# Performance work log

Measured on AMD Instinct MI355X. Metric: run time of the kernel, lower is better.

The kernel has to match this reference:

```python
import jax, jax.numpy as jnp
import numpy as np

B, T, I, H = 2048, 512, 9, 56


def _lstm_layer(x, w_ih, w_hh, b_ih, b_hh):
    """Single LSTM layer, batch_first x: [B, T, in] -> [B, T, H].
    PyTorch gate order: i, f, g, o."""
    # Precompute input projections for all timesteps in one GEMM: [B, T, 4H]
    xp = jnp.einsum('bti,gi->btg', x, w_ih) + b_ih + b_hh
    xp_t = jnp.transpose(xp, (1, 0, 2))  # [T, B, 4H]
    h0 = jnp.zeros((x.shape[0], w_hh.shape[1]), dtype=x.dtype)
    c0 = jnp.zeros_like(h0)

    def step(carry, xt):
        h, c = carry
        gates = xt + h @ w_hh.T  # [B, 4H]
        i, f, g, o = jnp.split(gates, 4, axis=-1)
        i = jax.nn.sigmoid(i)
        f = jax.nn.sigmoid(f)
        g = jnp.tanh(g)
        o = jax.nn.sigmoid(o)
        c = f * c + i * g
        h = o * jnp.tanh(c)
        return (h, c), h

    _, hs = jax.lax.scan(step, (h0, c0), xp_t)  # hs: [T, B, H]
    return jnp.transpose(hs, (1, 0, 2))  # [B, T, H]


def setup_inputs() -> dict:
    key = jax.random.key(0)
    ks = jax.random.split(key, 13)
    s_in = 1.0 / np.sqrt(H)
    inp = {
        'x': jax.random.normal(ks[0], (B, T, I), dtype=jnp.float32),
        'w_ih0': jax.random.uniform(ks[1], (4 * H, I), jnp.float32, -s_in, s_in),
        'w_hh0': jax.random.uniform(ks[2], (4 * H, H), jnp.float32, -s_in, s_in),
        'b_ih0': jax.random.uniform(ks[3], (4 * H,), jnp.float32, -s_in, s_in),
        'b_hh0': jax.random.uniform(ks[4], (4 * H,), jnp.float32, -s_in, s_in),
        'w_ih1': jax.random.uniform(ks[5], (4 * H, H), jnp.float32, -s_in, s_in),
        'w_hh1': jax.random.uniform(ks[6], (4 * H, H), jnp.float32, -s_in, s_in),
        'b_ih1': jax.random.uniform(ks[7], (4 * H,), jnp.float32, -s_in, s_in),
        'b_hh1': jax.random.uniform(ks[8], (4 * H,), jnp.float32, -s_in, s_in),
        'fc1_w': jax.random.uniform(ks[9], (H // 2, H), jnp.float32, -s_in, s_in),
        'fc1_b': jax.random.uniform(ks[10], (H // 2,), jnp.float32, -s_in, s_in),
        'fc2_w': jax.random.uniform(ks[11], (1, H // 2), jnp.float32, -0.2, 0.2),
        'fc2_b': jax.random.uniform(ks[12], (1,), jnp.float32, -0.2, 0.2),
    }
    return inp


def reference(x, w_ih0, w_hh0, b_ih0, b_hh0, w_ih1, w_hh1, b_ih1, b_hh1,
              fc1_w, fc1_b, fc2_w, fc2_b):
    h = _lstm_layer(x, w_ih0, w_hh0, b_ih0, b_hh0)   # [B, T, H]
    h = _lstm_layer(h, w_ih1, w_hh1, b_ih1, b_hh1)   # [B, T, H]
    last = h[:, -1]                                   # [B, H]
    y = jax.nn.relu(last @ fc1_w.T + fc1_b)           # [B, H//2]
    return y @ fc2_w.T + fc2_b                        # [B, 1]
```

## Files before the change

### kernel.cpp

```cpp
#include <hip/hip_runtime.h>
#include <stdint.h>

#define T_LEN 512
#define IN0   9
#define H     56
#define BG    8
#define NW    14
#define NTH   (NW * 64)
#define NBLK  256

typedef __attribute__((ext_vector_type(8))) short bfrag;
typedef __attribute__((ext_vector_type(4))) float ffrag;

#define MFMA(a,b,c) __builtin_amdgcn_mfma_f32_16x16x32_bf16((a),(b),(c),0,0,0)

__device__ __forceinline__ uint32_t bf16hi(float x) {
  uint32_t u = __float_as_uint(x);
  return (u + 0x7FFFu + ((u >> 16) & 1u)) & 0xFFFF0000u;
}
__device__ __forceinline__ void split_bf16(float x, short& hs, short& ls) {
  uint32_t hb = bf16hi(x);
  float lf = x - __uint_as_float(hb);
  hs = (short)(hb >> 16);
  ls = (short)(bf16hi(lf) >> 16);
}
__device__ __forceinline__ void split_bf16t(float x, short& hs, short& ls) {
  uint32_t hb = bf16hi(x);
  float lf = x - __uint_as_float(hb);
  hs = (short)(hb >> 16);
  ls = (short)(__float_as_uint(lf) >> 16);
}
__device__ __forceinline__ float dpp8_add(float v) {
  int p = __builtin_amdgcn_update_dpp(0, __float_as_int(v), 0x128, 0xF, 0xF, true);
  return v + __int_as_float(p);
}
__device__ __forceinline__ float rcp_f(float v)  { return __builtin_amdgcn_rcpf(v); }
__device__ __forceinline__ float sigm_f(float v) { return rcp_f(1.0f + __expf(-v)); }
__device__ __forceinline__ float tanh_f(float v) { return 1.0f - 2.0f * rcp_f(1.0f + __expf(2.0f * v)); }

__global__ __launch_bounds__(NTH, 4)
void lstm_mfma7(const float* __restrict__ x,
                const float* __restrict__ w_ih0, const float* __restrict__ w_hh0,
                const float* __restrict__ b_ih0, const float* __restrict__ b_hh0,
                const float* __restrict__ w_ih1, const float* __restrict__ w_hh1,
                const float* __restrict__ b_ih1, const float* __restrict__ b_hh1,
                const float* __restrict__ fc1_w, const float* __restrict__ fc1_b,
                const float* __restrict__ fc2_w, const float* __restrict__ fc2_b,
                float* __restrict__ out)
{
  __shared__ __align__(16) short sB[4][1024];
  __shared__ float sF[BG * H];
  __shared__ float sY[BG * 28];

  const int tid  = threadIdx.x;
  const int lane = tid & 63;
  const int w    = tid >> 6;
  const int c16  = lane & 15;
  const int quad = lane >> 4;

  const int np   = 16 * w + c16;
  const int jb   = np >> 2, gb = np & 3;
  const int wrow = gb * H + jb;

  for (int i = tid; i < (int)(sizeof(sB) / 4); i += NTH) ((int*)sB)[i] = 0;

  bfrag B0h[2], B0l[2], Buh[2], Bhh[2];
  #pragma unroll
  for (int s = 0; s < 2; ++s) {
    union { short sh[8]; bfrag v; } a0h, a0l, auh, ahh;
    #pragma unroll
    for (int jj = 0; jj < 8; ++jj) {
      const int k = 32 * s + quad * 8 + jj;
      const float w0 = (k < H) ? w_hh0[wrow * H + k] : w_ih0[wrow * IN0 + (k - 56)];
      const float wu = (k < H) ? w_ih1[wrow * H + k] : 0.0f;
      const float wh = (k < H) ? w_hh1[wrow * H + k] : 0.0f;
      split_bf16(w0, a0h.sh[jj], a0l.sh[jj]);
      short dum;
      split_bf16(wu, auh.sh[jj], dum);
      split_bf16(wh, ahh.sh[jj], dum);
    }
    B0h[s] = a0h.v; B0l[s] = a0l.v;
    Buh[s] = auh.v; Bhh[s] = ahh.v;
  }

  const int j4 = 4 * w + quad;
  ffrag bias0f, bias1f;
  #pragma unroll
  for (int r = 0; r < 4; ++r) {
    const float v0 = b_ih0[r * H + j4] + b_hh0[r * H + j4];
    const float v1 = b_ih1[r * H + j4] + b_hh1[r * H + j4];
    bias0f[r] = (c16 < 8) ? v0 : 0.0f;
    bias1f[r] = (c16 < 8) ? v1 : 0.0f;
  }
  const ffrag zerof = { 0.f, 0.f, 0.f, 0.f };

  const int lay = (lane >> 3) & 1;
  const int b   = lane & 7;
  float wx8a[4];
  #pragma unroll
  for (int r = 0; r < 4; ++r)
    wx8a[r] = lay ? w_ih0[(r * H + j4) * IN0 + 8] : 0.0f;

  const int kk   = j4 & 31;
  const int offE = (j4 >> 5) * 512 + ((kk >> 3) * 16 + b) * 8 + (kk & 7);
  short* const hp0 = &sB[0][0] + (lay ? 0 : 3 * 1024) + offE;
  short* const hp1 = &sB[0][0] + (lay ? 1 * 1024 : 2 * 1024) + offE;

  const int shalf = lane >> 5;
  const int sbq   = (lane >> 2) & 7;
  const int sjlc  = lane & 3;
  const int offX  = 512 + (48 + sbq) * 8 + 2 * sjlc;
  short* const xst0 = &sB[0][0] + offX;
  short* const xst1 = &sB[1][0] + offX;
  const short* const sBr = &sB[0][0];

  const float* xp8 = x + (size_t)(blockIdx.x * BG + b) * T_LEN * IN0 + 8;
  const float* xps = x + (size_t)(blockIdx.x * BG + sbq) * T_LEN * IN0
                   + (size_t)w * IN0 + 2 * sjlc;

  float cst = 0.f;
  __syncthreads();

  if (w == 0 && shalf) {
    const float xa = xps[0], xb = xps[1];
    short ah, al2, bh, bl2;
    split_bf16t(xa, ah, al2); split_bf16t(xb, bh, bl2);
    *(uint32_t*)xst0        = (uint16_t)ah  | ((uint32_t)(uint16_t)bh  << 16);
    *(uint32_t*)(xst0 + 64) = (uint16_t)al2 | ((uint32_t)(uint16_t)bl2 << 16);
    xps += 2 * IN0;
  }
  __syncthreads();

  {
    bfrag U0 = *(const bfrag*)(sBr + lane * 8);
    bfrag U1 = *(const bfrag*)(sBr + 512 + lane * 8);
    ffrag a0 = MFMA(B0h[0], U0, bias0f);
    a0 = MFMA(B0h[1], U1, a0);
    a0 = MFMA(B0l[0], U0, a0);
    a0 = MFMA(B0l[1], U1, a0);
    const float x8v = xp8[0];
    xp8 += IN0;
    float s0[4];
    #pragma unroll
    for (int r = 0; r < 4; ++r) s0[r] = dpp8_add(a0[r]);
    if (lay) {
      const float gi = fmaf(wx8a[0], x8v, s0[0]);
      const float gf = fmaf(wx8a[1], x8v, s0[1]);
      const float gg = fmaf(wx8a[2], x8v, s0[2]);
      const float go = fmaf(wx8a[3], x8v, s0[3]);
      const float iv = sigm_f(gi), fv = sigm_f(gf), gv = tanh_f(gg), ov = sigm_f(go);
      cst = fmaf(fv, cst, iv * gv);
      const float hv = ov * tanh_f(cst);
      short hs, hl; split_bf16t(hv, hs, hl);
      hp1[0] = hs; hp1[64] = hl;
    }
    if (w == 1 && shalf) {
      const float xa = xps[0], xb = xps[1];
      short ah, al2, bh, bl2;
      split_bf16t(xa, ah, al2); split_bf16t(xb, bh, bl2);
      *(uint32_t*)xst1        = (uint16_t)ah  | ((uint32_t)(uint16_t)bh  << 16);
      *(uint32_t*)(xst1 + 64) = (uint16_t)al2 | ((uint32_t)(uint16_t)bl2 << 16);
      xps += 2 * IN0;
    }
    __syncthreads();
  }

#define REGION(RR, L0PART, XSTG, LASTR)                                         \
  {                                                                             \
    bfrag U0 = *(const bfrag*)(sBr + (RR ^ 1) * 1024 + lane * 8);               \
    bfrag U1 = *(const bfrag*)(sBr + (RR ^ 1) * 1024 + 512 + lane * 8);         \
    bfrag H0 = *(const bfrag*)(sBr + (2 + RR) * 1024 + lane * 8);               \
    bfrag H1 = *(const bfrag*)(sBr + (2 + RR) * 1024 + 512 + lane * 8);         \
    float x8v = 0.0f;                                                           \
    if (L0PART) { x8v = xp8[0]; xp8 += IN0; }                                   \
                                     \
    ffrag a0;                                                                   \
    if (L0PART) {                                                               \
      a0 = MFMA(B0h[0], U0, bias0f);                                            \
      a0 = MFMA(B0h[1], U1, a0);                                                \
      a0 = MFMA(B0l[0], U0, a0);                                                \
      a0 = MFMA(B0l[1], U1, a0);                                                \
    }                                                                           \
                                                 \
    ffrag aH = MFMA(Bhh[0], H0, bias1f);                                        \
    aH = MFMA(Bhh[1], H1, aH);                                                  \
    ffrag aU = MFMA(Buh[0], U0, zerof);                                         \
    aU = MFMA(Buh[1], U1, aU);                                                  \
    if (!LASTR) {                                                               \
      float sv[4];                                                              \
      _Pragma("unroll")                                                         \
      for (int r = 0; r < 4; ++r) {                                             \
        const float s1 = dpp8_add(aH[r] + aU[r]);                               \
        const float s0 = dpp8_add(a0[r]);                                       \
        sv[r] = lay ? s0 : s1;                                                  \
      }                                                                         \
      const float gi = fmaf(wx8a[0], x8v, sv[0]);                               \
      const float gf = fmaf(wx8a[1], x8v, sv[1]);                               \
      const float gg = fmaf(wx8a[2], x8v, sv[2]);                               \
      const float go = fmaf(wx8a[3], x8v, sv[3]);                               \
      const float iv = sigm_f(gi), fv = sigm_f(gf);                             \
      const float gv = tanh_f(gg), ov = sigm_f(go);                             \
      cst = fmaf(fv, cst, iv * gv);                                             \
      const float hv = ov * tanh_f(cst);                                        \
      short hs, hl; split_bf16t(hv, hs, hl);                                    \
      short* hb = (RR == 0) ? hp0 : hp1;                                        \
      hb[0] = hs; hb[64] = hl;                                                  \
    } else {                                                                    \
      float s1[4];                                                              \
      _Pragma("unroll")                                                         \
      for (int r = 0; r < 4; ++r) s1[r] = dpp8_add(aH[r] + aU[r]);              \
      if (lay == 0) {                                                           \
        const float iv = sigm_f(s1[0]), fv = sigm_f(s1[1]);                     \
        const float gv = tanh_f(s1[2]), ov = sigm_f(s1[3]);                     \
        cst = fmaf(fv, cst, iv * gv);                                           \
        sF[b * H + j4] = ov * tanh_f(cst);                                      \
      }                                                                         \
    }                                                                           \
    if (XSTG) {                                                                 \
             \
      if (w == RR && shalf) {                                                   \
        const float xa = xps[0], xb = xps[1];                                   \
        short ah, al2, bh, bl2;                                                 \
        split_bf16t(xa, ah, al2); split_bf16t(xb, bh, bl2);                     \
        short* xb_ = (RR == 0) ? xst0 : xst1;                                   \
        *(uint32_t*)xb_        = (uint16_t)ah  | ((uint32_t)(uint16_t)bh  << 16); \
        *(uint32_t*)(xb_ + 64) = (uint16_t)al2 | ((uint32_t)(uint16_t)bl2 << 16); \
        xps += 2 * IN0;                                                         \
      }                                                                         \
    }                                                                           \
    __syncthreads();                                                            \
  }

  for (int it = 0; it < 255; ++it) {
    REGION(0, 1, 1, 0)
    REGION(1, 1, 1, 0)
  }
  REGION(0, 1, 0, 0)
  REGION(1, 0, 0, 1)
#undef REGION

  if (tid < 28 * BG) {
    const int m  = tid >> 3;
    const int bb = tid & 7;
    float acc = fc1_b[m];
    const float4* w4 = (const float4*)(fc1_w + m * H);
    const float4* h4 = (const float4*)(sF + bb * H);
    #pragma unroll
    for (int qq = 0; qq < H / 4; ++qq) {
      const float4 wv4 = w4[qq], hv4 = h4[qq];
      acc = fmaf(wv4.x, hv4.x, acc);
      acc = fmaf(wv4.y, hv4.y, acc);
      acc = fmaf(wv4.z, hv4.z, acc);
      acc = fmaf(wv4.w, hv4.w, acc);
    }
    sY[bb * 28 + m] = fmaxf(acc, 0.0f);
  }
  __syncthreads();
  if (tid < BG) {
    float acc = fc2_b[0];
    #pragma unroll
    for (int m = 0; m < 28; ++m)
      acc = fmaf(fc2_w[m], sY[tid * 28 + m], acc);
    out[blockIdx.x * BG + tid] = acc;
  }
}

extern "C" void kernel_launch(void* const* d_in, const int* in_sizes, int n_in,
                              void* d_out, int out_size, void* d_ws, size_t ws_size,
                              hipStream_t stream)
{
  const float* x     = (const float*)d_in[0];
  const float* w_ih0 = (const float*)d_in[1];
  const float* w_hh0 = (const float*)d_in[2];
  const float* b_ih0 = (const float*)d_in[3];
  const float* b_hh0 = (const float*)d_in[4];
  const float* w_ih1 = (const float*)d_in[5];
  const float* w_hh1 = (const float*)d_in[6];
  const float* b_ih1 = (const float*)d_in[7];
  const float* b_hh1 = (const float*)d_in[8];
  const float* fc1_w = (const float*)d_in[9];
  const float* fc1_b = (const float*)d_in[10];
  const float* fc2_w = (const float*)d_in[11];
  const float* fc2_b = (const float*)d_in[12];
  float* out = (float*)d_out;

  lstm_mfma7<<<NBLK, NTH, 0, stream>>>(
      x, w_ih0, w_hh0, b_ih0, b_hh0, w_ih1, w_hh1, b_ih1, b_hh1,
      fc1_w, fc1_b, fc2_w, fc2_b, out);
}
```

Measured before the change: 428.3 us.

## Prestage all input timesteps into LDS before the recurrent loop

Before the time loop, each block loads all 512 timesteps of its 8 batch rows from global memory, splits them into hi/lo bf16 parts and stores them in a large LDS buffer, with the ninth input feature kept as fp32 in a separate LDS array. The recurrent steps then read the x fragment and x8 value through pointers that advance through LDS. This removes the per-step global loads and the per-step staging of x by one wave. In exchange it uses almost all of the LDS and adds a serial prologue at the start of the kernel.

```diff
diff --git a/kernel.cpp b/kernel.cpp
--- a/kernel.cpp
+++ b/kernel.cpp
@@ -39,7 +39,7 @@
 __device__ __forceinline__ float tanh_f(float v) { return 1.0f - 2.0f * rcp_f(1.0f + __expf(2.0f * v)); }
 
 __global__ __launch_bounds__(NTH, 4)
-void lstm_mfma7(const float* __restrict__ x,
+void lstm_mfma9(const float* __restrict__ x,
                 const float* __restrict__ w_ih0, const float* __restrict__ w_hh0,
                 const float* __restrict__ b_ih0, const float* __restrict__ b_hh0,
                 const float* __restrict__ w_ih1, const float* __restrict__ w_hh1,
@@ -48,7 +48,9 @@
                 const float* __restrict__ fc2_w, const float* __restrict__ fc2_b,
                 float* __restrict__ out)
 {
-  __shared__ __align__(16) short sB[4][1024];
+  __shared__ __align__(16) short hbufS[4 * 1024];
+  __shared__ __align__(16) short xfS[T_LEN * 128];
+  __shared__ __align__(16) float x8S[T_LEN * BG];
   __shared__ float sF[BG * H];
   __shared__ float sY[BG * 28];
 
@@ -62,7 +64,7 @@
   const int jb   = np >> 2, gb = np & 3;
   const int wrow = gb * H + jb;
 
-  for (int i = tid; i < (int)(sizeof(sB) / 4); i += NTH) ((int*)sB)[i] = 0;
+  for (int i = tid; i < 2048; i += NTH) ((int*)hbufS)[i] = 0;
 
   bfrag B0h[2], B0l[2], Buh[2], Bhh[2];
   #pragma unroll
@@ -103,43 +105,49 @@
 
   const int kk   = j4 & 31;
   const int offE = (j4 >> 5) * 512 + ((kk >> 3) * 16 + b) * 8 + (kk & 7);
-  short* const hp0 = &sB[0][0] + (lay ? 0 : 3 * 1024) + offE;
-  short* const hp1 = &sB[0][0] + (lay ? 1 * 1024 : 2 * 1024) + offE;
-
-  const int shalf = lane >> 5;
-  const int sbq   = (lane >> 2) & 7;
-  const int sjlc  = lane & 3;
-  const int offX  = 512 + (48 + sbq) * 8 + 2 * sjlc;
-  short* const xst0 = &sB[0][0] + offX;
-  short* const xst1 = &sB[1][0] + offX;
-  const short* const sBr = &sB[0][0];
-
-  const float* xp8 = x + (size_t)(blockIdx.x * BG + b) * T_LEN * IN0 + 8;
-  const float* xps = x + (size_t)(blockIdx.x * BG + sbq) * T_LEN * IN0
-                   + (size_t)w * IN0 + 2 * sjlc;
+  short* const hp0 = hbufS + (lay ? 0 : 3 * 1024) + offE;
+  short* const hp1 = hbufS + (lay ? 1 * 1024 : 2 * 1024) + offE;
+
+  for (int item = tid; item < T_LEN * BG; item += NTH) {
+    const int t  = item & (T_LEN - 1);
+    const int bb = item >> 9;
+    const float* xr = x + ((size_t)(blockIdx.x * BG + bb) * T_LEN + t) * IN0;
+    union { short s[8]; bfrag v; } hi, lo;
+    #pragma unroll
+    for (int q = 0; q < 8; ++q) split_bf16t(xr[q], hi.s[q], lo.s[q]);
+    *(bfrag*)((char*)xfS + (size_t)t * 256 + bb * 16)       = hi.v;
+    *(bfrag*)((char*)xfS + (size_t)t * 256 + (bb + 8) * 16) = lo.v;
+    x8S[t * 8 + bb] = xr[8];
+  }
+
+  const char* const hB = (const char*)hbufS;
+  const char* const pU0_0 = hB + 2048 + lane * 16;
+  const char* const pU0_1 = hB +        lane * 16;
+  const char* const pH0_0 = hB + 4096 + lane * 16;
+  const char* const pH1_0 = hB + 5120 + lane * 16;
+  const char* const pH0_1 = hB + 6144 + lane * 16;
+  const char* const pH1_1 = hB + 7168 + lane * 16;
+  const char* pU1_0 = (quad == 3) ? ((const char*)xfS + 256 * 1 + c16 * 16)
+                                  : (hB + 3072 + lane * 16);
+  const char* pU1_1 = (quad == 3) ? ((const char*)xfS + 256 * 2 + c16 * 16)
+                                  : (hB + 1024 + lane * 16);
+  const char* px8_0 = (const char*)x8S + 32 * 1 + b * 4;
+  const char* px8_1 = (const char*)x8S + 32 * 2 + b * 4;
+  const int incU1 = (quad == 3) ? 512 : 0;
 
   float cst = 0.f;
   __syncthreads();
 
-  if (w == 0 && shalf) {
-    const float xa = xps[0], xb = xps[1];
-    short ah, al2, bh, bl2;
-    split_bf16t(xa, ah, al2); split_bf16t(xb, bh, bl2);
-    *(uint32_t*)xst0        = (uint16_t)ah  | ((uint32_t)(uint16_t)bh  << 16);
-    *(uint32_t*)(xst0 + 64) = (uint16_t)al2 | ((uint32_t)(uint16_t)bl2 << 16);
-    xps += 2 * IN0;
-  }
-  __syncthreads();
-
   {
-    bfrag U0 = *(const bfrag*)(sBr + lane * 8);
-    bfrag U1 = *(const bfrag*)(sBr + 512 + lane * 8);
+    const bfrag U0 = *(const bfrag*)(hB + lane * 16);
+    const char* pU1p = (quad == 3) ? ((const char*)xfS + c16 * 16)
+                                   : (hB + 1024 + lane * 16);
+    const bfrag U1 = *(const bfrag*)pU1p;
+    const float x8v = x8S[b];
     ffrag a0 = MFMA(B0h[0], U0, bias0f);
     a0 = MFMA(B0h[1], U1, a0);
     a0 = MFMA(B0l[0], U0, a0);
     a0 = MFMA(B0l[1], U1, a0);
-    const float x8v = xp8[0];
-    xp8 += IN0;
     float s0[4];
     #pragma unroll
     for (int r = 0; r < 4; ++r) s0[r] = dpp8_add(a0[r]);
@@ -148,34 +156,26 @@
       const float gf = fmaf(wx8a[1], x8v, s0[1]);
       const float gg = fmaf(wx8a[2], x8v, s0[2]);
       const float go = fmaf(wx8a[3], x8v, s0[3]);
-      const float iv = sigm_f(gi), fv = sigm_f(gf), gv = tanh_f(gg), ov = sigm_f(go);
+      const float iv = sigm_f(gi), fv = sigm_f(gf);
+      const float gv = tanh_f(gg), ov = sigm_f(go);
       cst = fmaf(fv, cst, iv * gv);
       const float hv = ov * tanh_f(cst);
       short hs, hl; split_bf16t(hv, hs, hl);
       hp1[0] = hs; hp1[64] = hl;
     }
-    if (w == 1 && shalf) {
-      const float xa = xps[0], xb = xps[1];
-      short ah, al2, bh, bl2;
-      split_bf16t(xa, ah, al2); split_bf16t(xb, bh, bl2);
-      *(uint32_t*)xst1        = (uint16_t)ah  | ((uint32_t)(uint16_t)bh  << 16);
-      *(uint32_t*)(xst1 + 64) = (uint16_t)al2 | ((uint32_t)(uint16_t)bl2 << 16);
-      xps += 2 * IN0;
-    }
     __syncthreads();
   }
 
-#define REGION(RR, L0PART, XSTG, LASTR)                                         \
+#define REGION(RR, L0PART, LASTR)                                               \
   {                                                                             \
-    bfrag U0 = *(const bfrag*)(sBr + (RR ^ 1) * 1024 + lane * 8);               \
-    bfrag U1 = *(const bfrag*)(sBr + (RR ^ 1) * 1024 + 512 + lane * 8);         \
-    bfrag H0 = *(const bfrag*)(sBr + (2 + RR) * 1024 + lane * 8);               \
-    bfrag H1 = *(const bfrag*)(sBr + (2 + RR) * 1024 + 512 + lane * 8);         \
+    const bfrag U0 = *(const bfrag*)pU0_##RR;                                   \
+    const bfrag U1 = *(const bfrag*)pU1_##RR;                                   \
+    const bfrag H0 = *(const bfrag*)pH0_##RR;                                   \
+    const bfrag H1 = *(const bfrag*)pH1_##RR;                                   \
+    ffrag a0;                                                                   \
     float x8v = 0.0f;                                                           \
-    if (L0PART) { x8v = xp8[0]; xp8 += IN0; }                                   \
-                                     \
-    ffrag a0;                                                                   \
     if (L0PART) {                                                               \
+      x8v = *(const float*)px8_##RR;                                            \
       a0 = MFMA(B0h[0], U0, bias0f);                                            \
       a0 = MFMA(B0h[1], U1, a0);                                                \
       a0 = MFMA(B0l[0], U0, a0);                                                \
@@ -203,8 +203,8 @@
       cst = fmaf(fv, cst, iv * gv);                                             \
       const float hv = ov * tanh_f(cst);                                        \
       short hs, hl; split_bf16t(hv, hs, hl);                                    \
-      short* hb = (RR == 0) ? hp0 : hp1;                                        \
-      hb[0] = hs; hb[64] = hl;                                                  \
+      short* hb2 = (RR == 0) ? hp0 : hp1;                                       \
+      hb2[0] = hs; hb2[64] = hl;                                                \
     } else {                                                                    \
       float s1[4];                                                              \
       _Pragma("unroll")                                                         \
@@ -216,27 +216,18 @@
         sF[b * H + j4] = ov * tanh_f(cst);                                      \
       }                                                                         \
     }                                                                           \
-    if (XSTG) {                                                                 \
-             \
-      if (w == RR && shalf) {                                                   \
-        const float xa = xps[0], xb = xps[1];                                   \
-        short ah, al2, bh, bl2;                                                 \
-        split_bf16t(xa, ah, al2); split_bf16t(xb, bh, bl2);                     \
-        short* xb_ = (RR == 0) ? xst0 : xst1;                                   \
-        *(uint32_t*)xb_        = (uint16_t)ah  | ((uint32_t)(uint16_t)bh  << 16); \
-        *(uint32_t*)(xb_ + 64) = (uint16_t)al2 | ((uint32_t)(uint16_t)bl2 << 16); \
-        xps += 2 * IN0;                                                         \
-      }                                                                         \
-    }                                                                           \
     __syncthreads();                                                            \
   }
 
   for (int it = 0; it < 255; ++it) {
-    REGION(0, 1, 1, 0)
-    REGION(1, 1, 1, 0)
-  }
-  REGION(0, 1, 0, 0)
-  REGION(1, 0, 0, 1)
+    REGION(0, 1, 0)
+    REGION(1, 1, 0)
+    pU1_0 += incU1; pU1_1 += incU1;
+    px8_0 += 64;    px8_1 += 64;
+  }
+  REGION(0, 1, 0)
+  pU1_1 -= incU1;
+  REGION(1, 0, 1)
 #undef REGION
 
   if (tid < 28 * BG) {
@@ -284,7 +275,7 @@
   const float* fc2_b = (const float*)d_in[12];
   float* out = (float*)d_out;
 
-  lstm_mfma7<<<NBLK, NTH, 0, stream>>>(
+  lstm_mfma9<<<NBLK, NTH, 0, stream>>>(
       x, w_ih0, w_hh0, b_ih0, b_hh0, w_ih1, w_hh1, b_ih1, b_hh1,
       fc1_w, fc1_b, fc2_w, fc2_b, out);
 }
```

After: 434.3 us. About the same (+1.4%).
